# Performance work log

Measured on AMD Instinct MI355X. Metric: run time of the kernel, lower is better.

The kernel has to match this reference:

```python
import jax, jax.numpy as jnp
import numpy as np

DIM = 128
HOP = 2
NEIGH = [12, 2]  # neighbor_num per hop
ALPHA = 0.2      # leaky-relu slope
NUM_NODE = 50000
B, S = 128, 50
STDV = 1.0 / np.sqrt(DIM)


def _leaky(x):
    return jnp.where(x >= 0, x, ALPHA * x)


def _local_agg(h, adj, a_local):
    # h: [B,S,D], adj: [B,S,S] ints in 0..4, a_local: [4,D]
    a_in = h[:, :, None, :] * h[:, None, :, :]            # [B,S,S,D]
    e = _leaky(jnp.einsum('bijd,kd->kbij', a_in, a_local))  # [4,B,S,S]
    att = jnp.full(adj.shape, -9e15, dtype=h.dtype)
    for k in range(4):
        att = jnp.where(adj == k + 1, e[k], att)
    att = jax.nn.softmax(att, axis=-1)
    return jnp.einsum('bij,bjd->bid', att, h)


def _global_agg(self_v, neigh_v, extra_v, w1, w2, w3, bias):
    # self_v: [B,N,D], neigh_v: [B,N,K,D], extra_v: [B,N,D]
    a = _leaky(jnp.einsum('bnkd,de->bnke', extra_v[:, :, None, :] * neigh_v, w1))
    a = jnp.einsum('bnke,e->bnk', a, w2)
    a = jax.nn.softmax(a, axis=-1)
    agg = jnp.einsum('bnk,bnkd->bnd', a, neigh_v)
    out = jnp.concatenate([self_v, agg], axis=-1) @ w3 + bias
    return jax.nn.relu(out)


def setup_inputs() -> dict:
    key = jax.random.key(0)
    ks = jax.random.split(key, 12)
    u = lambda k, shp: jax.random.uniform(k, shp, jnp.float32, -STDV, STDV)
    return {
        'inputs': jax.random.randint(ks[0], (B, S), 0, NUM_NODE),
        'adj': jax.random.randint(ks[1], (B, S, S), 0, 5),
        'mask_item': jnp.ones((B, S), dtype=jnp.int32),
        'item': jax.random.randint(ks[2], (B, S), 0, NUM_NODE),
        'first_adj': jax.random.randint(ks[3], (B, S * NEIGH[0]), 0, NUM_NODE),
        'adj_all': jax.random.randint(ks[4], (NUM_NODE, 2), 0, NUM_NODE),
        'embedding': u(ks[5], (NUM_NODE, DIM)),
        'a_local': u(ks[6], (4, DIM)),
        'gw1': u(ks[7], (HOP, DIM, DIM)),
        'gw2': u(ks[8], (HOP, DIM)),
        'gw3': u(ks[9], (HOP, 2 * DIM, DIM)),
        'gbias': u(ks[10], (HOP, DIM)),
    }


def reference(inputs, adj, mask_item, item, first_adj, adj_all,
              embedding, a_local, gw1, gw2, gw3, gbias):
    b, s = inputs.shape
    h = embedding[inputs]                                  # [B,S,D]
    h_local = _local_agg(h, adj, a_local)

    m = mask_item.astype(embedding.dtype)[..., None]       # [B,S,1]
    item_emb = embedding[item] * m
    sum_item = jnp.sum(item_emb, 1) / jnp.sum(m, 1)        # [B,D]
    sess = sum_item[:, None, :]                            # [B,1,D]

    # multi-hop neighbor sampling
    neigh1 = first_adj.reshape(b, s * NEIGH[0])            # [B, 600]
    neigh2 = adj_all[neigh1.reshape(-1)].reshape(b, s * NEIGH[0] * NEIGH[1])  # [B,1200]
    ev = [embedding[inputs], embedding[neigh1], embedding[neigh2]]

    for n_hop in range(HOP):
        nxt = []
        for hop in range(HOP - n_hop):
            neigh_v = ev[hop + 1].reshape(b, -1, NEIGH[hop], DIM)
            extra_v = jnp.broadcast_to(sess, (b, ev[hop].shape[1], DIM))
            nxt.append(_global_agg(ev[hop], neigh_v, extra_v,
                                   gw1[n_hop], gw2[n_hop], gw3[n_hop], gbias[n_hop]))
        ev = nxt
    h_global = ev[0].reshape(b, s, DIM)

    # dropout is identity at eval
    return h_local + h_global
```

## Files before the change

kernel.cpp:

```cpp
#include <hip/hip_runtime.h>
#include <stdint.h>

typedef unsigned short ushort_t;
typedef __attribute__((ext_vector_type(8))) short bf16x8;
typedef __attribute__((ext_vector_type(4))) float f32x4;

#define B_   128
#define S_   50
#define D_   128
#define ALPHA_ 0.2f

__device__ __forceinline__ float bf2f(ushort_t u){
  return __uint_as_float(((uint32_t)u) << 16);
}
__device__ __forceinline__ ushort_t f2bf(float f){
  uint32_t x = __float_as_uint(f);
  x = (x + 0x7fffu + ((x >> 16) & 1u)) >> 16;
  return (ushort_t)x;
}
__device__ __forceinline__ float leaky(float x){ return x >= 0.f ? x : ALPHA_*x; }

__global__ void detect_kernel(const uint32_t* __restrict__ emb_raw, int* __restrict__ flag){
  if (threadIdx.x == 0 && blockIdx.x == 0){
    int ok = 1;
    for (int i = 0; i < 64; i++){
      uint32_t lo = emb_raw[i] & 0xffffu;
      uint32_t ex = (lo >> 7) & 0xFFu;
      if (!(lo == 0u || (ex >= 64u && ex <= 126u))) ok = 0;
    }
    *flag = ok;
  }
}

__global__ void cvt_all(const void* __restrict__ p0, const void* __restrict__ p1,
                        const void* __restrict__ p2, const void* __restrict__ p3,
                        const void* __restrict__ p4, const void* __restrict__ p5,
                        ushort_t* __restrict__ dst, const int* __restrict__ flag){
  const int seg_end[6] = {6400000, 6400512, 6433280, 6433536, 6499072, 6499328};
  int base = (blockIdx.x*256 + threadIdx.x) * 4;
  if (base >= 6499328) return;
  int s = 0;
  while (base >= seg_end[s]) s++;
  int segbase = (s == 0) ? 0 : seg_end[s-1];
  const void* src = (s==0)?p0:(s==1)?p1:(s==2)?p2:(s==3)?p3:(s==4)?p4:p5;
  int off = base - segbase;
  union { ushort_t u[4]; uint2 d2; } o;
  if (*flag){
    o.d2 = *(const uint2*)((const ushort_t*)src + off);
  } else {
    float4 v = *(const float4*)((const float*)src + off);
    o.u[0] = f2bf(v.x); o.u[1] = f2bf(v.y); o.u[2] = f2bf(v.z); o.u[3] = f2bf(v.w);
  }
  *(uint2*)(dst + base) = o.d2;
}

__global__ void sess_kernel(const int* __restrict__ item, const int* __restrict__ mask,
                            const ushort_t* __restrict__ emb, ushort_t* __restrict__ sessb){
  int b = blockIdx.x, d = threadIdx.x;
  float acc = 0.f, den = 0.f;
  for (int s = 0; s < S_; s++){
    float fm = (float)mask[b*S_ + s];
    int id = item[b*S_ + s];
    acc += fm * bf2f(emb[(size_t)id*D_ + d]);
    den += fm;
  }
  sessb[b*D_ + d] = f2bf(acc / den);
}

__global__ __launch_bounds__(256) void local_mfma2(
    const int* __restrict__ inputs, const int* __restrict__ adj,
    const ushort_t* __restrict__ emb, const ushort_t* __restrict__ alocb,
    ushort_t* __restrict__ hlb){
  __shared__ ushort_t hS[64][136];
  __shared__ float    attS[16][68];
  __shared__ int      sids[64];
  int blk = blockIdx.x;
  int b  = blk >> 2;
  int mi = blk & 3;
  int tid = threadIdx.x;
  if (tid < 64) sids[tid] = (tid < S_) ? inputs[b*S_ + tid] : 0;
  __syncthreads();
  for (int idx = tid; idx < 64*16; idx += 256){
    int j = idx >> 4, ch = idx & 15;
    uint4 v = {0u, 0u, 0u, 0u};
    if (j < S_) v = *(const uint4*)(emb + (size_t)sids[j]*D_ + ch*8);
    *(uint4*)(&hS[j][ch*8]) = v;
  }
  for (int idx = tid; idx < 16*64; idx += 256)
    attS[idx >> 6][idx & 63] = -9.0e15f;
  __syncthreads();

  int lane = tid & 63, wv = tid >> 6;
  int q = lane >> 4, c = lane & 15;

  f32x4 Eacc[4];
  #pragma unroll
  for (int ni = 0; ni < 4; ni++) Eacc[ni] = (f32x4){0.f,0.f,0.f,0.f};
  #pragma unroll
  for (int kt = 0; kt < 4; kt++){
    uint4 av = *(const uint4*)(alocb + wv*D_ + kt*32 + q*8);
    const uint32_t* ap = (const uint32_t*)&av;
    uint4 hv = *(const uint4*)(&hS[mi*16 + c][kt*32 + q*8]);
    const uint32_t* hp = (const uint32_t*)&hv;
    union { ushort_t u[8]; bf16x8 v; } afr;
    #pragma unroll
    for (int p = 0; p < 4; p++){
      float x0 = __uint_as_float(hp[p] << 16)         * __uint_as_float(ap[p] << 16);
      float x1 = __uint_as_float(hp[p] & 0xffff0000u) * __uint_as_float(ap[p] & 0xffff0000u);
      afr.u[2*p]   = f2bf(x0);
      afr.u[2*p+1] = f2bf(x1);
    }
    #pragma unroll
    for (int ni = 0; ni < 4; ni++){
      union { uint4 q4; bf16x8 v; } bfr;
      bfr.q4 = *(const uint4*)(&hS[ni*16 + c][kt*32 + q*8]);
      Eacc[ni] = __builtin_amdgcn_mfma_f32_16x16x32_bf16(afr.v, bfr.v, Eacc[ni], 0,0,0);
    }
  }
  const int* adjb = adj + (size_t)b*S_*S_;
  #pragma unroll
  for (int ni = 0; ni < 4; ni++){
    int j = ni*16 + c;
    #pragma unroll
    for (int r = 0; r < 4; r++){
      int i = mi*16 + q*4 + r;
      if (i < S_ && j < S_){
        int kk = adjb[i*S_ + j];
        if (kk == wv + 1) attS[q*4 + r][j] = leaky(Eacc[ni][r]);
      }
    }
  }
  __syncthreads();
  if (tid < 16){
    int i = mi*16 + tid;
    if (i < S_){
      float mx = -__builtin_inff();
      for (int j = 0; j < S_; j++) mx = fmaxf(mx, attS[tid][j]);
      float s = 0.f;
      for (int j = 0; j < S_; j++){ float e = __expf(attS[tid][j] - mx); attS[tid][j] = e; s += e; }
      float inv = 1.f / s;
      for (int j = 0; j < S_; j++) attS[tid][j] *= inv;
      for (int j = S_; j < 64; j++) attS[tid][j] = 0.f;
    } else {
      for (int j = 0; j < 64; j++) attS[tid][j] = 0.f;
    }
  }
  __syncthreads();
  f32x4 Pacc[2];
  Pacc[0] = (f32x4){0.f,0.f,0.f,0.f};
  Pacc[1] = (f32x4){0.f,0.f,0.f,0.f};
  #pragma unroll
  for (int kt = 0; kt < 2; kt++){
    union { ushort_t u[8]; bf16x8 v; } afr;
    const float* arow = &attS[c][kt*32 + q*8];
    #pragma unroll
    for (int j = 0; j < 8; j++) afr.u[j] = f2bf(arow[j]);
    #pragma unroll
    for (int nn = 0; nn < 2; nn++){
      int ni = 2*wv + nn;
      union { ushort_t u[8]; bf16x8 v; } bfr;
      #pragma unroll
      for (int jj = 0; jj < 8; jj++)
        bfr.u[jj] = hS[kt*32 + q*8 + jj][ni*16 + c];
      Pacc[nn] = __builtin_amdgcn_mfma_f32_16x16x32_bf16(afr.v, bfr.v, Pacc[nn], 0,0,0);
    }
  }
  #pragma unroll
  for (int nn = 0; nn < 2; nn++){
    int d = (2*wv + nn)*16 + c;
    #pragma unroll
    for (int r = 0; r < 4; r++){
      int i = mi*16 + q*4 + r;
      if (i < S_) hlb[((size_t)b*S_ + i)*D_ + d] = f2bf(Pacc[nn][r]);
    }
  }
}

__global__ __launch_bounds__(256) void score_mfma_ab(
    const ushort_t* __restrict__ sessb, const ushort_t* __restrict__ emb,
    const int* __restrict__ neigh1, const int* __restrict__ adj_all,
    const ushort_t* __restrict__ w1, const ushort_t* __restrict__ w2,
    float* __restrict__ score, int nA){
  __shared__ uint4 bfrag[2048];
  int tid = threadIdx.x;
  for (int idx = tid; idx < 2048; idx += 256){
    int kt = idx >> 9, rem = idx & 511, t = rem >> 6, ln = rem & 63;
    int qq = ln >> 4, cc = ln & 15;
    union { ushort_t u[8]; uint4 q4; } e;
    #pragma unroll
    for (int j = 0; j < 8; j++)
      e.u[j] = w1[(32*kt + qq*8 + j)*128 + 16*t + cc];
    bfrag[idx] = e.q4;
  }
  __syncthreads();
  int lane = tid & 63, wave = tid >> 6;
  int m = lane & 15, q = lane >> 4;
  float w2v[8];
  #pragma unroll
  for (int t = 0; t < 8; t++) w2v[t] = bf2f(w2[16*t + m]);

  for (int it = 0; it < 2; it++){
    int row_base = blockIdx.x*128 + it*64 + wave*16;
    int row = row_base + m;
    const ushort_t* nrow; int b;
    if (row < nA){
      nrow = emb + (size_t)neigh1[row]*D_;
      b = row / 600;
    } else {
      int r2 = row - nA;
      nrow = emb + (size_t)adj_all[(size_t)neigh1[r2>>1]*2 + (r2&1)]*D_;
      b = r2 / 1200;
    }
    const ushort_t* srow = sessb + (size_t)b*D_;

    f32x4 acc[8];
    #pragma unroll
    for (int t = 0; t < 8; t++) acc[t] = (f32x4){0.f,0.f,0.f,0.f};
    #pragma unroll
    for (int kt = 0; kt < 4; kt++){
      uint4 nv = *(const uint4*)(nrow + kt*32 + q*8);
      uint4 sv = *(const uint4*)(srow + kt*32 + q*8);
      const uint32_t* np = (const uint32_t*)&nv;
      const uint32_t* sp = (const uint32_t*)&sv;
      union { ushort_t u[8]; bf16x8 v; } afr;
      #pragma unroll
      for (int p = 0; p < 4; p++){
        uint32_t n2 = np[p], s2 = sp[p];
        float a0 = __uint_as_float(n2 << 16)          * __uint_as_float(s2 << 16);
        float a1 = __uint_as_float(n2 & 0xffff0000u)  * __uint_as_float(s2 & 0xffff0000u);
        afr.u[2*p]   = f2bf(a0);
        afr.u[2*p+1] = f2bf(a1);
      }
      #pragma unroll
      for (int t = 0; t < 8; t++){
        union { uint4 q4; bf16x8 v; } bfr;
        bfr.q4 = bfrag[(kt*8 + t)*64 + lane];
        acc[t] = __builtin_amdgcn_mfma_f32_16x16x32_bf16(afr.v, bfr.v, acc[t], 0, 0, 0);
      }
    }
    #pragma unroll
    for (int r = 0; r < 4; r++){
      float s = 0.f;
      #pragma unroll
      for (int t = 0; t < 8; t++) s += leaky(acc[t][r]) * w2v[t];
      s += __shfl_xor(s, 1, 64);
      s += __shfl_xor(s, 2, 64);
      s += __shfl_xor(s, 4, 64);
      s += __shfl_xor(s, 8, 64);
      if (m == 0) score[row_base + q*4 + r] = s;
    }
  }
}

__global__ __launch_bounds__(256) void score_mfma_c(
    const ushort_t* __restrict__ sessb, const ushort_t* __restrict__ out1,
    const ushort_t* __restrict__ w1, const ushort_t* __restrict__ w2,
    float* __restrict__ score){
  __shared__ uint4 bfrag[2048];
  int tid = threadIdx.x;
  for (int idx = tid; idx < 2048; idx += 256){
    int kt = idx >> 9, rem = idx & 511, t = rem >> 6, ln = rem & 63;
    int qq = ln >> 4, cc = ln & 15;
    union { ushort_t u[8]; uint4 q4; } e;
    #pragma unroll
    for (int j = 0; j < 8; j++)
      e.u[j] = w1[(32*kt + qq*8 + j)*128 + 16*t + cc];
    bfrag[idx] = e.q4;
  }
  __syncthreads();
  int lane = tid & 63, wave = tid >> 6;
  int m = lane & 15, q = lane >> 4;
  float w2v[8];
  #pragma unroll
  for (int t = 0; t < 8; t++) w2v[t] = bf2f(w2[16*t + m]);
  for (int it = 0; it < 2; it++){
    int row_base = blockIdx.x*128 + it*64 + wave*16;
    int row = row_base + m;
    const ushort_t* nrow = out1 + (size_t)row*D_;
    int b = row / 600;
    const ushort_t* srow = sessb + (size_t)b*D_;
    f32x4 acc[8];
    #pragma unroll
    for (int t = 0; t < 8; t++) acc[t] = (f32x4){0.f,0.f,0.f,0.f};
    #pragma unroll
    for (int kt = 0; kt < 4; kt++){
      uint4 nv = *(const uint4*)(nrow + kt*32 + q*8);
      uint4 sv = *(const uint4*)(srow + kt*32 + q*8);
      const uint32_t* np = (const uint32_t*)&nv;
      const uint32_t* sp = (const uint32_t*)&sv;
      union { ushort_t u[8]; bf16x8 v; } afr;
      #pragma unroll
      for (int p = 0; p < 4; p++){
        uint32_t n2 = np[p], s2 = sp[p];
        float a0 = __uint_as_float(n2 << 16)          * __uint_as_float(s2 << 16);
        float a1 = __uint_as_float(n2 & 0xffff0000u)  * __uint_as_float(s2 & 0xffff0000u);
        afr.u[2*p]   = f2bf(a0);
        afr.u[2*p+1] = f2bf(a1);
      }
      #pragma unroll
      for (int t = 0; t < 8; t++){
        union { uint4 q4; bf16x8 v; } bfr;
        bfr.q4 = bfrag[(kt*8 + t)*64 + lane];
        acc[t] = __builtin_amdgcn_mfma_f32_16x16x32_bf16(afr.v, bfr.v, acc[t], 0, 0, 0);
      }
    }
    #pragma unroll
    for (int r = 0; r < 4; r++){
      float s = 0.f;
      #pragma unroll
      for (int t = 0; t < 8; t++) s += leaky(acc[t][r]) * w2v[t];
      s += __shfl_xor(s, 1, 64);
      s += __shfl_xor(s, 2, 64);
      s += __shfl_xor(s, 4, 64);
      s += __shfl_xor(s, 8, 64);
      if (m == 0) score[row_base + q*4 + r] = s;
    }
  }
}

template<int K>
__device__ __forceinline__ void softmaxK(const float* __restrict__ sc, float att[K]){
  float mx = -__builtin_inff();
  #pragma unroll
  for (int k = 0; k < K; k++){ att[k] = sc[k]; mx = fmaxf(mx, att[k]); }
  float s = 0.f;
  #pragma unroll
  for (int k = 0; k < K; k++){ att[k] = __expf(att[k] - mx); s += att[k]; }
  float inv = 1.f / s;
  #pragma unroll
  for (int k = 0; k < K; k++) att[k] *= inv;
}

template<int K, int NT>
__device__ __forceinline__ void out_tile(
    int lane, const uint4* __restrict__ afrag,
    const ushort_t* __restrict__ sptr, const ushort_t* const nptr[K],
    const float att[K], f32x4 acc[NT]){
  int q = lane >> 4;
  #pragma unroll
  for (int kt = 0; kt < 8; kt++){
    union { ushort_t u[8]; uint4 q4; bf16x8 v; } bfr;
    if (kt < 4){
      bfr.q4 = *(const uint4*)(sptr + kt*32 + q*8);
    } else {
      float g[8] = {0,0,0,0,0,0,0,0};
      #pragma unroll
      for (int k = 0; k < K; k++){
        uint4 nv = *(const uint4*)(nptr[k] + (kt-4)*32 + q*8);
        const uint32_t* np = (const uint32_t*)&nv;
        #pragma unroll
        for (int p = 0; p < 4; p++){
          g[2*p]   = fmaf(att[k], __uint_as_float(np[p] << 16),         g[2*p]);
          g[2*p+1] = fmaf(att[k], __uint_as_float(np[p] & 0xffff0000u), g[2*p+1]);
        }
      }
      #pragma unroll
      for (int j = 0; j < 8; j++) bfr.u[j] = f2bf(g[j]);
    }
    #pragma unroll
    for (int t = 0; t < NT; t++){
      union { uint4 q4; bf16x8 v; } af;
      af.q4 = afrag[(kt*NT + t)*64 + lane];
      acc[t] = __builtin_amdgcn_mfma_f32_16x16x32_bf16(af.v, bfr.v, acc[t], 0, 0, 0);
    }
  }
}

__global__ __launch_bounds__(256) void out_mfma_ab(
    const float* __restrict__ score, const int* __restrict__ idx,
    const int* __restrict__ nbr, const int* __restrict__ adj_all,
    const ushort_t* __restrict__ emb,
    const ushort_t* __restrict__ w3, const ushort_t* __restrict__ bias,
    ushort_t* __restrict__ o0c, ushort_t* __restrict__ out1c,
    int nA, int nTot, int scoreBbase){
  __shared__ uint4 afrag[2048];
  int half = blockIdx.x & 1;
  int rb   = blockIdx.x >> 1;
  int tbase = half*4;
  int tid = threadIdx.x;
  for (int i = tid; i < 2048; i += 256){
    int kt = i >> 8, rem = i & 255, t = rem >> 6, ln = rem & 63;
    int qq = ln >> 4, cc = ln & 15;
    union { ushort_t u[8]; uint4 q4; } e;
    #pragma unroll
    for (int j = 0; j < 8; j++)
      e.u[j] = w3[(32*kt + qq*8 + j)*128 + 16*(tbase + t) + cc];
    afrag[i] = e.q4;
  }
  __syncthreads();
  int lane = tid & 63, wave = tid >> 6;
  int mrow = lane & 15, q = lane >> 4;
  float bv[4][4];
  #pragma unroll
  for (int t = 0; t < 4; t++){
    const ushort_t* bp = bias + 16*(tbase + t) + q*4;
    #pragma unroll
    for (int r = 0; r < 4; r++) bv[t][r] = bf2f(bp[r]);
  }
  for (int it = 0; it < 2; it++){
    int row_base = rb*128 + it*64 + wave*16;
    int row = row_base + mrow;
    bool active = row < nTot;
    int rowc = active ? row : (nTot - 1);
    bool isA = rowc < nA;
    f32x4 acc[4];
    #pragma unroll
    for (int t = 0; t < 4; t++) acc[t] = (f32x4){0.f,0.f,0.f,0.f};
    if (isA){
      const ushort_t* sptr = emb + (size_t)idx[rowc]*D_;
      const ushort_t* nptr[12];
      #pragma unroll
      for (int k = 0; k < 12; k++) nptr[k] = emb + (size_t)nbr[rowc*12 + k]*D_;
      float att[12];
      softmaxK<12>(score + (size_t)rowc*12, att);
      out_tile<12,4>(lane, afrag, sptr, nptr, att, acc);
    } else {
      int rB = rowc - nA;
      const ushort_t* sptr = emb + (size_t)nbr[rB]*D_;
      const ushort_t* nptr[2];
      #pragma unroll
      for (int k = 0; k < 2; k++) nptr[k] = emb + (size_t)adj_all[(size_t)nbr[rB]*2 + k]*D_;
      float att[2];
      softmaxK<2>(score + scoreBbase + (size_t)rB*2, att);
      out_tile<2,4>(lane, afrag, sptr, nptr, att, acc);
    }
    if (active){
      ushort_t* dst = isA ? (o0c + (size_t)row*D_) : (out1c + (size_t)(row - nA)*D_);
      #pragma unroll
      for (int t = 0; t < 4; t++){
        int col0 = 16*(tbase + t) + q*4;
        union { ushort_t u[4]; uint2 d2; } pk;
        #pragma unroll
        for (int r = 0; r < 4; r++) pk.u[r] = f2bf(fmaxf(acc[t][r] + bv[t][r], 0.f));
        *(uint2*)(dst + col0) = pk.d2;
      }
    }
  }
}

__global__ __launch_bounds__(256) void out_mfma_c(
    const float* __restrict__ score, const ushort_t* __restrict__ out1,
    const ushort_t* __restrict__ selfsrc,
    const ushort_t* __restrict__ w3, const ushort_t* __restrict__ bias,
    const ushort_t* __restrict__ addsrc, float* __restrict__ outf, int nrows){
  __shared__ uint4 afrag[4096];
  int tid = threadIdx.x;
  for (int i = tid; i < 4096; i += 256){
    int kt = i >> 9, rem = i & 511, t = rem >> 6, ln = rem & 63;
    int qq = ln >> 4, cc = ln & 15;
    union { ushort_t u[8]; uint4 q4; } e;
    #pragma unroll
    for (int j = 0; j < 8; j++)
      e.u[j] = w3[(32*kt + qq*8 + j)*128 + 16*t + cc];
    afrag[i] = e.q4;
  }
  __syncthreads();
  int lane = tid & 63, wave = tid >> 6;
  int mrow = lane & 15, q = lane >> 4;
  float bv[8][4];
  #pragma unroll
  for (int t = 0; t < 8; t++){
    const ushort_t* bp = bias + 16*t + q*4;
    #pragma unroll
    for (int r = 0; r < 4; r++) bv[t][r] = bf2f(bp[r]);
  }
  for (int it = 0; it < 2; it++){
    int row_base = blockIdx.x*128 + it*64 + wave*16;
    int row = row_base + mrow;
    bool active = row < nrows;
    int rowc = active ? row : (nrows - 1);
    const ushort_t* sptr = selfsrc + (size_t)rowc*D_;
    const ushort_t* nptr[12];
    #pragma unroll
    for (int k = 0; k < 12; k++) nptr[k] = out1 + (size_t)(rowc*12 + k)*D_;
    float att[12];
    softmaxK<12>(score + (size_t)rowc*12, att);
    f32x4 acc[8];
    #pragma unroll
    for (int t = 0; t < 8; t++) acc[t] = (f32x4){0.f,0.f,0.f,0.f};
    out_tile<12,8>(lane, afrag, sptr, nptr, att, acc);
    if (active){
      #pragma unroll
      for (int t = 0; t < 8; t++){
        int col0 = 16*t + q*4;
        float v[4];
        const ushort_t* ap = addsrc + (size_t)row*D_ + col0;
        #pragma unroll
        for (int r = 0; r < 4; r++)
          v[r] = fmaxf(acc[t][r] + bv[t][r], 0.f) + bf2f(ap[r]);
        *(f32x4*)(outf + (size_t)row*D_ + col0) = (f32x4){v[0], v[1], v[2], v[3]};
      }
    }
  }
}

extern "C" void kernel_launch(void* const* d_in, const int* in_sizes, int n_in,
                              void* d_out, int out_size, void* d_ws, size_t ws_size,
                              hipStream_t stream) {
  const int* inputs    = (const int*)d_in[0];
  const int* adj       = (const int*)d_in[1];
  const int* mask_item = (const int*)d_in[2];
  const int* item      = (const int*)d_in[3];
  const int* first_adj = (const int*)d_in[4];
  const int* adj_all   = (const int*)d_in[5];

  char* ws = (char*)d_ws;
  size_t o = 0;
  int*      flag   = (int*)(ws + o);      o += 64;
  ushort_t* emb_b  = (ushort_t*)(ws + o); o += 12800000;
  ushort_t* alocb  = (ushort_t*)(ws + o); o += 1024;
  ushort_t* gw1b   = (ushort_t*)(ws + o); o += 65536;
  ushort_t* gw2b   = (ushort_t*)(ws + o); o += 512;
  ushort_t* gw3b   = (ushort_t*)(ws + o); o += 131072;
  ushort_t* gbb    = (ushort_t*)(ws + o); o += 512;
  ushort_t* sessb  = (ushort_t*)(ws + o); o += 32768;
  ushort_t* hlb    = (ushort_t*)(ws + o); o += 1638400;
  size_t fixed = o;
  int CHB = 16;
  if      (ws_size >= fixed + (size_t)128*173600) CHB = 128;
  else if (ws_size >= fixed + (size_t)64 *173600) CHB = 64;
  else if (ws_size >= fixed + (size_t)32 *173600) CHB = 32;
  ushort_t* out1c = (ushort_t*)(ws + o);  o += (size_t)CHB*153600;
  ushort_t* o0c   = (ushort_t*)(ws + o);  o += (size_t)CHB*12800;
  float*    score = (float*)(ws + o);

  float* outp = (float*)d_out;

  detect_kernel<<<1, 64, 0, stream>>>((const uint32_t*)d_in[6], flag);
  cvt_all<<<(6499328/4 + 255)/256, 256, 0, stream>>>(d_in[6], d_in[7], d_in[8], d_in[9],
                                                     d_in[10], d_in[11], emb_b, flag);

  sess_kernel<<<B_, 128, 0, stream>>>(item, mask_item, emb_b, sessb);
  local_mfma2<<<B_*4, 256, 0, stream>>>(inputs, adj, emb_b, alocb, hlb);

  int nchunk = B_ / CHB;
  for (int c = 0; c < nchunk; c++){
    int b0 = c * CHB;
    const int* fadj  = first_adj + (size_t)b0 * 600;
    const ushort_t* sbc = sessb + (size_t)b0 * D_;
    ushort_t*  hlc   = hlb  + (size_t)b0 * 50 * D_;
    float*     outc  = outp + (size_t)b0 * 50 * D_;
    int nA600 = CHB*600, nA50 = CHB*50, nTot = CHB*650;

    score_mfma_ab<<<(3*nA600)/128, 256, 0, stream>>>(sbc, emb_b, fadj, adj_all,
                                                     gw1b, gw2b, score, nA600);
    out_mfma_ab<<<((nTot + 127)/128)*2, 256, 0, stream>>>(score, inputs + b0*50, fadj, adj_all,
                                                          emb_b, gw3b, gbb, o0c, out1c,
                                                          nA50, nTot, nA600);
    score_mfma_c<<<nA600/128, 256, 0, stream>>>(sbc, out1c, gw1b + 16384, gw2b + 128, score);
    out_mfma_c<<<(nA50 + 127)/128, 256, 0, stream>>>(score, out1c, o0c,
                                                     gw3b + 32768, gbb + 128,
                                                     hlc, outc, nA50);
  }
}
```

Before: 218.1 us.

## Precompute MFMA weight fragments globally instead of per-block LDS staging

```diff
diff --git a/kernel.cpp b/kernel.cpp
--- a/kernel.cpp
+++ b/kernel.cpp
@@ -54,6 +54,34 @@
   *(uint2*)(dst + base) = o.d2;
 }
 
+__global__ void prep_frags(const ushort_t* __restrict__ w1, const ushort_t* __restrict__ w3,
+                           uint4* __restrict__ w1f, uint4* __restrict__ w3f){
+  int id = blockIdx.x*256 + threadIdx.x;
+  if (id >= 12288) return;
+  if (id < 4096){
+    int h = id >> 11, i = id & 2047;
+    int kt = i >> 9, rem = i & 511, t = rem >> 6, ln = rem & 63;
+    int q = ln >> 4, c = ln & 15;
+    const ushort_t* w = w1 + h*16384;
+    union { ushort_t u[8]; uint4 q4; } e;
+    #pragma unroll
+    for (int j = 0; j < 8; j++)
+      e.u[j] = w[(32*kt + q*8 + j)*128 + 16*t + c];
+    w1f[h*2048 + i] = e.q4;
+  } else {
+    int id2 = id - 4096;
+    int h = id2 >> 12, i = id2 & 4095;
+    int kt = i >> 9, rem = i & 511, t = rem >> 6, ln = rem & 63;
+    int q = ln >> 4, c = ln & 15;
+    const ushort_t* w = w3 + h*32768;
+    union { ushort_t u[8]; uint4 q4; } e;
+    #pragma unroll
+    for (int j = 0; j < 8; j++)
+      e.u[j] = w[(32*kt + q*8 + j)*128 + 16*t + c];
+    w3f[h*4096 + i] = e.q4;
+  }
+}
+
 __global__ void sess_kernel(const int* __restrict__ item, const int* __restrict__ mask,
                             const ushort_t* __restrict__ emb, ushort_t* __restrict__ sessb){
   int b = blockIdx.x, d = threadIdx.x;
@@ -179,20 +207,9 @@
 __global__ __launch_bounds__(256) void score_mfma_ab(
     const ushort_t* __restrict__ sessb, const ushort_t* __restrict__ emb,
     const int* __restrict__ neigh1, const int* __restrict__ adj_all,
-    const ushort_t* __restrict__ w1, const ushort_t* __restrict__ w2,
+    const uint4* __restrict__ w1f, const ushort_t* __restrict__ w2,
     float* __restrict__ score, int nA){
-  __shared__ uint4 bfrag[2048];
   int tid = threadIdx.x;
-  for (int idx = tid; idx < 2048; idx += 256){
-    int kt = idx >> 9, rem = idx & 511, t = rem >> 6, ln = rem & 63;
-    int qq = ln >> 4, cc = ln & 15;
-    union { ushort_t u[8]; uint4 q4; } e;
-    #pragma unroll
-    for (int j = 0; j < 8; j++)
-      e.u[j] = w1[(32*kt + qq*8 + j)*128 + 16*t + cc];
-    bfrag[idx] = e.q4;
-  }
-  __syncthreads();
   int lane = tid & 63, wave = tid >> 6;
   int m = lane & 15, q = lane >> 4;
   float w2v[8];
@@ -234,7 +251,7 @@
       #pragma unroll
       for (int t = 0; t < 8; t++){
         union { uint4 q4; bf16x8 v; } bfr;
-        bfr.q4 = bfrag[(kt*8 + t)*64 + lane];
+        bfr.q4 = w1f[(kt*8 + t)*64 + lane];
         acc[t] = __builtin_amdgcn_mfma_f32_16x16x32_bf16(afr.v, bfr.v, acc[t], 0, 0, 0);
       }
     }
@@ -254,20 +271,9 @@
 
 __global__ __launch_bounds__(256) void score_mfma_c(
     const ushort_t* __restrict__ sessb, const ushort_t* __restrict__ out1,
-    const ushort_t* __restrict__ w1, const ushort_t* __restrict__ w2,
+    const uint4* __restrict__ w1f, const ushort_t* __restrict__ w2,
     float* __restrict__ score){
-  __shared__ uint4 bfrag[2048];
   int tid = threadIdx.x;
-  for (int idx = tid; idx < 2048; idx += 256){
-    int kt = idx >> 9, rem = idx & 511, t = rem >> 6, ln = rem & 63;
-    int qq = ln >> 4, cc = ln & 15;
-    union { ushort_t u[8]; uint4 q4; } e;
-    #pragma unroll
-    for (int j = 0; j < 8; j++)
-      e.u[j] = w1[(32*kt + qq*8 + j)*128 + 16*t + cc];
-    bfrag[idx] = e.q4;
-  }
-  __syncthreads();
   int lane = tid & 63, wave = tid >> 6;
   int m = lane & 15, q = lane >> 4;
   float w2v[8];
@@ -300,7 +306,7 @@
       #pragma unroll
       for (int t = 0; t < 8; t++){
         union { uint4 q4; bf16x8 v; } bfr;
-        bfr.q4 = bfrag[(kt*8 + t)*64 + lane];
+        bfr.q4 = w1f[(kt*8 + t)*64 + lane];
         acc[t] = __builtin_amdgcn_mfma_f32_16x16x32_bf16(afr.v, bfr.v, acc[t], 0, 0, 0);
       }
     }
@@ -331,11 +337,11 @@
   for (int k = 0; k < K; k++) att[k] *= inv;
 }
 
-template<int K, int NT>
+template<int K>
 __device__ __forceinline__ void out_tile(
-    int lane, const uint4* __restrict__ afrag,
+    int lane, const uint4* __restrict__ w3f,
     const ushort_t* __restrict__ sptr, const ushort_t* const nptr[K],
-    const float att[K], f32x4 acc[NT]){
+    const float att[K], f32x4 acc[8]){
   int q = lane >> 4;
   #pragma unroll
   for (int kt = 0; kt < 8; kt++){
@@ -358,9 +364,9 @@
       for (int j = 0; j < 8; j++) bfr.u[j] = f2bf(g[j]);
     }
     #pragma unroll
-    for (int t = 0; t < NT; t++){
+    for (int t = 0; t < 8; t++){
       union { uint4 q4; bf16x8 v; } af;
-      af.q4 = afrag[(kt*NT + t)*64 + lane];
+      af.q4 = w3f[(kt*8 + t)*64 + lane];
       acc[t] = __builtin_amdgcn_mfma_f32_16x16x32_bf16(af.v, bfr.v, acc[t], 0, 0, 0);
     }
   }
@@ -369,43 +375,29 @@
 __global__ __launch_bounds__(256) void out_mfma_ab(
     const float* __restrict__ score, const int* __restrict__ idx,
     const int* __restrict__ nbr, const int* __restrict__ adj_all,
-    const ushort_t* __restrict__ emb,
-    const ushort_t* __restrict__ w3, const ushort_t* __restrict__ bias,
+    const ushort_t* __restrict__ emb, const uint4* __restrict__ w3f,
+    const ushort_t* __restrict__ bias,
     ushort_t* __restrict__ o0c, ushort_t* __restrict__ out1c,
     int nA, int nTot, int scoreBbase){
-  __shared__ uint4 afrag[2048];
-  int half = blockIdx.x & 1;
-  int rb   = blockIdx.x >> 1;
-  int tbase = half*4;
   int tid = threadIdx.x;
-  for (int i = tid; i < 2048; i += 256){
-    int kt = i >> 8, rem = i & 255, t = rem >> 6, ln = rem & 63;
-    int qq = ln >> 4, cc = ln & 15;
-    union { ushort_t u[8]; uint4 q4; } e;
-    #pragma unroll
-    for (int j = 0; j < 8; j++)
-      e.u[j] = w3[(32*kt + qq*8 + j)*128 + 16*(tbase + t) + cc];
-    afrag[i] = e.q4;
-  }
-  __syncthreads();
   int lane = tid & 63, wave = tid >> 6;
   int mrow = lane & 15, q = lane >> 4;
-  float bv[4][4];
-  #pragma unroll
-  for (int t = 0; t < 4; t++){
-    const ushort_t* bp = bias + 16*(tbase + t) + q*4;
+  float bv[8][4];
+  #pragma unroll
+  for (int t = 0; t < 8; t++){
+    const ushort_t* bp = bias + 16*t + q*4;
     #pragma unroll
     for (int r = 0; r < 4; r++) bv[t][r] = bf2f(bp[r]);
   }
   for (int it = 0; it < 2; it++){
-    int row_base = rb*128 + it*64 + wave*16;
+    int row_base = blockIdx.x*128 + it*64 + wave*16;
     int row = row_base + mrow;
     bool active = row < nTot;
     int rowc = active ? row : (nTot - 1);
     bool isA = rowc < nA;
-    f32x4 acc[4];
-    #pragma unroll
-    for (int t = 0; t < 4; t++) acc[t] = (f32x4){0.f,0.f,0.f,0.f};
+    f32x4 acc[8];
+    #pragma unroll
+    for (int t = 0; t < 8; t++) acc[t] = (f32x4){0.f,0.f,0.f,0.f};
     if (isA){
       const ushort_t* sptr = emb + (size_t)idx[rowc]*D_;
       const ushort_t* nptr[12];
@@ -413,7 +405,7 @@
       for (int k = 0; k < 12; k++) nptr[k] = emb + (size_t)nbr[rowc*12 + k]*D_;
       float att[12];
       softmaxK<12>(score + (size_t)rowc*12, att);
-      out_tile<12,4>(lane, afrag, sptr, nptr, att, acc);
+      out_tile<12>(lane, w3f, sptr, nptr, att, acc);
     } else {
       int rB = rowc - nA;
       const ushort_t* sptr = emb + (size_t)nbr[rB]*D_;
@@ -422,13 +414,13 @@
       for (int k = 0; k < 2; k++) nptr[k] = emb + (size_t)adj_all[(size_t)nbr[rB]*2 + k]*D_;
       float att[2];
       softmaxK<2>(score + scoreBbase + (size_t)rB*2, att);
-      out_tile<2,4>(lane, afrag, sptr, nptr, att, acc);
+      out_tile<2>(lane, w3f, sptr, nptr, att, acc);
     }
     if (active){
       ushort_t* dst = isA ? (o0c + (size_t)row*D_) : (out1c + (size_t)(row - nA)*D_);
       #pragma unroll
-      for (int t = 0; t < 4; t++){
-        int col0 = 16*(tbase + t) + q*4;
+      for (int t = 0; t < 8; t++){
+        int col0 = 16*t + q*4;
         union { ushort_t u[4]; uint2 d2; } pk;
         #pragma unroll
         for (int r = 0; r < 4; r++) pk.u[r] = f2bf(fmaxf(acc[t][r] + bv[t][r], 0.f));
@@ -440,21 +432,10 @@
 
 __global__ __launch_bounds__(256) void out_mfma_c(
     const float* __restrict__ score, const ushort_t* __restrict__ out1,
-    const ushort_t* __restrict__ selfsrc,
-    const ushort_t* __restrict__ w3, const ushort_t* __restrict__ bias,
+    const ushort_t* __restrict__ selfsrc, const uint4* __restrict__ w3f,
+    const ushort_t* __restrict__ bias,
     const ushort_t* __restrict__ addsrc, float* __restrict__ outf, int nrows){
-  __shared__ uint4 afrag[4096];
   int tid = threadIdx.x;
-  for (int i = tid; i < 4096; i += 256){
-    int kt = i >> 9, rem = i & 511, t = rem >> 6, ln = rem & 63;
-    int qq = ln >> 4, cc = ln & 15;
-    union { ushort_t u[8]; uint4 q4; } e;
-    #pragma unroll
-    for (int j = 0; j < 8; j++)
-      e.u[j] = w3[(32*kt + qq*8 + j)*128 + 16*t + cc];
-    afrag[i] = e.q4;
-  }
-  __syncthreads();
   int lane = tid & 63, wave = tid >> 6;
   int mrow = lane & 15, q = lane >> 4;
   float bv[8][4];
@@ -478,7 +459,7 @@
     f32x4 acc[8];
     #pragma unroll
     for (int t = 0; t < 8; t++) acc[t] = (f32x4){0.f,0.f,0.f,0.f};
-    out_tile<12,8>(lane, afrag, sptr, nptr, att, acc);
+    out_tile<12>(lane, w3f, sptr, nptr, att, acc);
     if (active){
       #pragma unroll
       for (int t = 0; t < 8; t++){
@@ -515,6 +496,8 @@
   ushort_t* gbb    = (ushort_t*)(ws + o); o += 512;
   ushort_t* sessb  = (ushort_t*)(ws + o); o += 32768;
   ushort_t* hlb    = (ushort_t*)(ws + o); o += 1638400;
+  uint4*    w1f    = (uint4*)(ws + o);    o += 65536;
+  uint4*    w3f    = (uint4*)(ws + o);    o += 131072;
   size_t fixed = o;
   int CHB = 16;
   if      (ws_size >= fixed + (size_t)128*173600) CHB = 128;
@@ -529,6 +512,7 @@
   detect_kernel<<<1, 64, 0, stream>>>((const uint32_t*)d_in[6], flag);
   cvt_all<<<(6499328/4 + 255)/256, 256, 0, stream>>>(d_in[6], d_in[7], d_in[8], d_in[9],
                                                      d_in[10], d_in[11], emb_b, flag);
+  prep_frags<<<48, 256, 0, stream>>>(gw1b, gw3b, w1f, w3f);
 
   sess_kernel<<<B_, 128, 0, stream>>>(item, mask_item, emb_b, sessb);
   local_mfma2<<<B_*4, 256, 0, stream>>>(inputs, adj, emb_b, alocb, hlb);
@@ -543,13 +527,13 @@
     int nA600 = CHB*600, nA50 = CHB*50, nTot = CHB*650;
 
     score_mfma_ab<<<(3*nA600)/128, 256, 0, stream>>>(sbc, emb_b, fadj, adj_all,
-                                                     gw1b, gw2b, score, nA600);
-    out_mfma_ab<<<((nTot + 127)/128)*2, 256, 0, stream>>>(score, inputs + b0*50, fadj, adj_all,
-                                                          emb_b, gw3b, gbb, o0c, out1c,
-                                                          nA50, nTot, nA600);
-    score_mfma_c<<<nA600/128, 256, 0, stream>>>(sbc, out1c, gw1b + 16384, gw2b + 128, score);
+                                                     w1f, gw2b, score, nA600);
+    out_mfma_ab<<<(nTot + 127)/128, 256, 0, stream>>>(score, inputs + b0*50, fadj, adj_all,
+                                                      emb_b, w3f, gbb, o0c, out1c,
+                                                      nA50, nTot, nA600);
+    score_mfma_c<<<nA600/128, 256, 0, stream>>>(sbc, out1c, w1f + 2048, gw2b + 128, score);
     out_mfma_c<<<(nA50 + 127)/128, 256, 0, stream>>>(score, out1c, o0c,
-                                                     gw3b + 32768, gbb + 128,
+                                                     w3f + 4096, gbb + 128,
                                                      hlc, outc, nA50);
   }
 }
```

New measurement: 285.2 us. 1.31x slower.
